# Kernel tuning notes

Hardware: AMD Instinct MI355X
Metric: run time of the kernel (lower is better)

## Reference

```python
import jax, jax.numpy as jnp
import numpy as np

N_NODES = 50000
N_EDGES = 800000
IN_C, HID_C, OUT_C, HEADS = 128, 32, 64, 8
NEG_SLOPE = 0.2


def gat_layer(x, src, dst, W, a_src, a_dst, bias, concat, num_nodes):
    # W: [F_in, H*C]; a_src, a_dst: [H, C]; bias: [H*C] or [C]
    H, C = a_src.shape
    h = (x @ W).reshape(num_nodes, H, C)                      # [N,H,C]
    e_src = (h * a_src).sum(-1)                               # [N,H]
    e_dst = (h * a_dst).sum(-1)                               # [N,H]
    e = jax.nn.leaky_relu(e_src[src] + e_dst[dst], NEG_SLOPE) # [E,H]
    # segment softmax over incoming edges of each destination node
    m = jax.ops.segment_max(e, dst, num_segments=num_nodes)   # [N,H]
    ex = jnp.exp(e - m[dst])
    den = jax.ops.segment_sum(ex, dst, num_segments=num_nodes)
    alpha = ex / (den[dst] + 1e-16)                           # [E,H]
    out = jax.ops.segment_sum(h[src] * alpha[..., None], dst, num_segments=num_nodes)  # [N,H,C]
    out = out.reshape(num_nodes, H * C) if concat else out.mean(axis=1)
    return out + bias


def setup_inputs() -> dict:
    key = jax.random.key(0)
    ks = jax.random.split(key, 10)
    x = jax.random.normal(ks[0], (N_NODES, IN_C), dtype=jnp.float32)
    edge_index = jax.random.randint(ks[1], (2, N_EDGES), 0, N_NODES, dtype=jnp.int64)
    s1 = (2.0 / (IN_C + HID_C * HEADS)) ** 0.5
    s2 = (2.0 / (HID_C * HEADS + OUT_C)) ** 0.5
    return {
        "x": x,
        "edge_index": edge_index,
        "W1": jax.random.normal(ks[2], (IN_C, HEADS * HID_C), dtype=jnp.float32) * s1,
        "a_src1": jax.random.normal(ks[3], (HEADS, HID_C), dtype=jnp.float32) * 0.1,
        "a_dst1": jax.random.normal(ks[4], (HEADS, HID_C), dtype=jnp.float32) * 0.1,
        "b1": jnp.zeros((HEADS * HID_C,), dtype=jnp.float32),
        "W2": jax.random.normal(ks[5], (HEADS * HID_C, OUT_C), dtype=jnp.float32) * s2,
        "a_src2": jax.random.normal(ks[6], (1, OUT_C), dtype=jnp.float32) * 0.1,
        "a_dst2": jax.random.normal(ks[7], (1, OUT_C), dtype=jnp.float32) * 0.1,
        "b2": jnp.zeros((OUT_C,), dtype=jnp.float32),
    }


def reference(x, edge_index, W1, a_src1, a_dst1, b1, W2, a_src2, a_dst2, b2):
    # add self-loops (PyG GATConv default)
    loops = jnp.arange(N_NODES, dtype=edge_index.dtype)
    src = jnp.concatenate([edge_index[0], loops])
    dst = jnp.concatenate([edge_index[1], loops])
    # dropout layers are identity in eval mode
    h = gat_layer(x, src, dst, W1, a_src1, a_dst1, b1, True, N_NODES)
    h = jax.nn.elu(h)
    out = gat_layer(h, src, dst, W2, a_src2, a_dst2, b2, False, N_NODES)
    return out
```

## Files before the change

kernel.cpp:

```cpp
#include <hip/hip_runtime.h>
#include <math.h>

#define N_NODES 50000
#define N_EDGES 800000
#define E_TOT   850000
#define IN_C    128
#define HID_C   32
#define OUT_C   64
#define HEADS   8
#define F1      256
#define PAD     64
#define NDUMMY  1024
#define G1_BLOCKS 3125
#define CSR_BLOCKS 782

typedef __bf16 bf16x8 __attribute__((ext_vector_type(8)));
typedef float  f32x4  __attribute__((ext_vector_type(4)));
typedef float  f32x2  __attribute__((ext_vector_type(2)));
typedef unsigned short us8 __attribute__((ext_vector_type(8)));

__device__ __forceinline__ unsigned short f2b(float f) {
    unsigned u = __float_as_uint(f);
    u += 0x7FFF + ((u >> 16) & 1);
    return (unsigned short)(u >> 16);
}
__device__ __forceinline__ float b2f(unsigned short b) {
    return __uint_as_float(((unsigned)b) << 16);
}
__device__ __forceinline__ float blo(unsigned u) { return __uint_as_float(u << 16); }
__device__ __forceinline__ float bhi(unsigned u) { return __uint_as_float(u & 0xffff0000u); }
__device__ __forceinline__ f32x2 up2(unsigned u) {
    f32x2 r; r.x = blo(u); r.y = bhi(u); return r;
}

__global__ void convert_w(const float* __restrict__ W1, const float* __restrict__ W2,
                          const float* __restrict__ a_src2, const float* __restrict__ a_dst2,
                          unsigned short* __restrict__ W1t, unsigned short* __restrict__ W2t,
                          float* __restrict__ w2s, float* __restrict__ w2d,
                          int* __restrict__ deg, unsigned short* __restrict__ ssrc) {
    int gid = blockIdx.x * 256 + threadIdx.x;
    if (gid < N_NODES) {
        deg[gid] = 1;
        ssrc[gid * PAD] = (unsigned short)gid;
    } else if (gid < N_NODES + NDUMMY) {
        deg[gid] = 0;
    }
    if (gid < 256) {
        float s = 0.f, dd = 0.f;
        for (int c = 0; c < OUT_C; c++) {
            float w = W2[gid * OUT_C + c];
            s  += w * a_src2[c];
            dd += w * a_dst2[c];
        }
        w2s[gid] = s; w2d[gid] = dd;
    }
    if (gid < 256 * 128) {
        int n = gid >> 7, k = gid & 127;
        W1t[gid] = f2b(W1[k * F1 + n]);
    } else if (gid < 256 * 128 + 64 * 256) {
        int o = gid - 256 * 128;
        int n = o >> 8, k = o & 255;
        W2t[o] = f2b(W2[k * OUT_C + n]);
    }
}

__global__ __launch_bounds__(256) void g1csr(const float* __restrict__ x,
                                             const unsigned short* __restrict__ W1t,
                                             const float* __restrict__ a_src,
                                             const float* __restrict__ a_dst,
                                             unsigned short* __restrict__ h1b,
                                             float* __restrict__ e_src,
                                             float* __restrict__ e_dst,
                                             const int* __restrict__ ei,
                                             int* __restrict__ deg,
                                             unsigned short* __restrict__ ssrc) {
    if (blockIdx.x >= G1_BLOCKS) {
        int e0 = (blockIdx.x - G1_BLOCKS) * 1024 + threadIdx.x;
        int s[4], d[4], p[4];
#pragma unroll
        for (int j = 0; j < 4; j++) {
            int e = e0 + j * 256;
            int le = (e < N_EDGES) ? e : (N_EDGES - 1);
            int es = ei[le];
            int ed = ei[N_EDGES + le];
            s[j] = es;
            d[j] = (e < N_EDGES) ? ed : (N_NODES + (e - N_EDGES));
        }
#pragma unroll
        for (int j = 0; j < 4; j++) p[j] = atomicAdd(&deg[d[j]], 1);
#pragma unroll
        for (int j = 0; j < 4; j++) ssrc[d[j] * PAD + p[j]] = (unsigned short)s[j];
        return;
    }
    const int t = threadIdx.x;
    const int wave = t >> 6, lane = t & 63;
    const int mlane = lane & 15, quad = lane >> 4;
    const int row0 = blockIdx.x * 16;
    const int col0 = wave * 64;
    const float* xr = x + (size_t)(row0 + mlane) * IN_C;
    bf16x8 afr[4];
#pragma unroll
    for (int kc = 0; kc < 4; kc++) {
        float4 f0 = *(const float4*)&xr[kc * 32 + quad * 8];
        float4 f1 = *(const float4*)&xr[kc * 32 + quad * 8 + 4];
        us8 u;
        u[0] = f2b(f0.x); u[1] = f2b(f0.y); u[2] = f2b(f0.z); u[3] = f2b(f0.w);
        u[4] = f2b(f1.x); u[5] = f2b(f1.y); u[6] = f2b(f1.z); u[7] = f2b(f1.w);
        afr[kc] = __builtin_bit_cast(bf16x8, u);
    }
    f32x4 c[4];
#pragma unroll
    for (int nt = 0; nt < 4; nt++) c[nt] = (f32x4){0.f, 0.f, 0.f, 0.f};
#pragma unroll
    for (int kc = 0; kc < 4; kc++) {
#pragma unroll
        for (int nt = 0; nt < 4; nt++) {
            int col = col0 + nt * 16 + mlane;
            uint4 bw = *(const uint4*)&W1t[(size_t)col * IN_C + kc * 32 + quad * 8];
            bf16x8 b = __builtin_bit_cast(bf16x8, bw);
            c[nt] = __builtin_amdgcn_mfma_f32_16x16x32_bf16(afr[kc], b, c[nt], 0, 0, 0);
        }
    }
#pragma unroll
    for (int nt = 0; nt < 4; nt++) {
#pragma unroll
        for (int r = 0; r < 4; r++) {
            int gr = row0 + quad * 4 + r;
            h1b[(size_t)gr * F1 + col0 + nt * 16 + mlane] = f2b(c[nt][r]);
        }
    }
    float asA0 = a_src[col0 + mlane],      asA1 = a_src[col0 + 16 + mlane];
    float asB0 = a_src[col0 + 32 + mlane], asB1 = a_src[col0 + 48 + mlane];
    float adA0 = a_dst[col0 + mlane],      adA1 = a_dst[col0 + 16 + mlane];
    float adB0 = a_dst[col0 + 32 + mlane], adB1 = a_dst[col0 + 48 + mlane];
#pragma unroll
    for (int r = 0; r < 4; r++) {
        float psA = c[0][r] * asA0 + c[1][r] * asA1;
        float pdA = c[0][r] * adA0 + c[1][r] * adA1;
        float psB = c[2][r] * asB0 + c[3][r] * asB1;
        float pdB = c[2][r] * adB0 + c[3][r] * adB1;
#pragma unroll
        for (int off = 1; off < 16; off <<= 1) {
            psA += __shfl_xor(psA, off, 64);
            pdA += __shfl_xor(pdA, off, 64);
            psB += __shfl_xor(psB, off, 64);
            pdB += __shfl_xor(pdB, off, 64);
        }
        if (mlane == 0) {
            int gr = row0 + quad * 4 + r;
            e_src[gr * HEADS + wave * 2]     = psA;
            e_src[gr * HEADS + wave * 2 + 1] = psB;
            e_dst[gr * HEADS + wave * 2]     = pdA;
            e_dst[gr * HEADS + wave * 2 + 1] = pdB;
        }
    }
}

__global__ __launch_bounds__(256) void agg1s(const unsigned short* __restrict__ h1b,
                                             const float* __restrict__ e_src,
                                             const float* __restrict__ e_dst,
                                             const int* __restrict__ deg,
                                             const unsigned short* __restrict__ ssrc,
                                             const float* __restrict__ b1,
                                             const float* __restrict__ w2s,
                                             const float* __restrict__ w2d,
                                             unsigned short* __restrict__ hhb,
                                             float* __restrict__ e_src2,
                                             float* __restrict__ e_dst2) {
    int v = (blockIdx.x * 256 + threadIdx.x) >> 6;
    int lane = threadIdx.x & 63;
    int half = lane >> 5, l32 = lane & 31;
    int c0 = l32 * 8, h_acc = l32 >> 2;
    int c2 = c0 << 1;
    int h_exp = l32 & 7, j_exp = l32 >> 3;
    const char* h1c = (const char*)h1b;
    const char* esc = (const char*)e_src;
    int d = deg[v];
    int beg = v * PAD;
    int s_all = (int)ssrc[beg + lane];
    float edh = e_dst[v * HEADS + h_exp];
    f32x2 acc[4];
#pragma unroll
    for (int k = 0; k < 4; k++) acc[k] = (f32x2){0.f, 0.f};
    float den = 0.f;
    int dm1 = d - 1;
    for (int k16 = 0; k16 < d; k16 += 16) {
        int slotA = k16 + half + 2 * j_exp;
        int slotB = slotA + 8;
        int sA = __shfl(s_all, (slotA < dm1 ? slotA : dm1), 64);
        int sB = __shfl(s_all, (slotB < dm1 ? slotB : dm1), 64);
        float eA = *(const float*)(esc + ((sA << 5) + (h_exp << 2))) + edh;
        float eB = *(const float*)(esc + ((sB << 5) + (h_exp << 2))) + edh;
        eA = fmaxf(eA, 0.2f * eA);
        eB = fmaxf(eB, 0.2f * eB);
        float wA = (slotA < d) ? __expf(eA) : 0.f;
        float wB = (slotB < d) ? __expf(eB) : 0.f;
        int s_j[8];
#pragma unroll
        for (int j = 0; j < 8; j++) {
            int slot = k16 + half + 2 * j;
            s_j[j] = __shfl(s_all, (slot < dm1 ? slot : dm1), 64);
        }
        float w_j[8];
#pragma unroll
        for (int j = 0; j < 4; j++) {
            w_j[j]     = __shfl(wA, (j << 3) | h_acc, 32);
            w_j[j + 4] = __shfl(wB, (j << 3) | h_acc, 32);
        }
        uint4 r[8];
#pragma unroll
        for (int j = 0; j < 8; j++)
            r[j] = *(const uint4*)(h1c + (((unsigned)s_j[j] << 9) + c2));
#pragma unroll
        for (int j = 0; j < 8; j++) {
            den += w_j[j];
            acc[0] += w_j[j] * up2(r[j].x);
            acc[1] += w_j[j] * up2(r[j].y);
            acc[2] += w_j[j] * up2(r[j].z);
            acc[3] += w_j[j] * up2(r[j].w);
        }
    }
    den += __shfl_xor(den, 32, 64);
#pragma unroll
    for (int k = 0; k < 4; k++) {
        acc[k].x += __shfl_xor(acc[k].x, 32, 64);
        acc[k].y += __shfl_xor(acc[k].y, 32, 64);
    }
    if (half == 0) {
        float dinv = 1.f / (den + 1e-16f);
        us8 o;
        float ps = 0.f, pd = 0.f;
#pragma unroll
        for (int k = 0; k < 4; k++) {
            float v0 = acc[k].x * dinv + b1[c0 + 2 * k];
            float v1 = acc[k].y * dinv + b1[c0 + 2 * k + 1];
            v0 = (v0 > 0.f) ? v0 : (__expf(v0) - 1.f);
            v1 = (v1 > 0.f) ? v1 : (__expf(v1) - 1.f);
            o[2 * k]     = f2b(v0);
            o[2 * k + 1] = f2b(v1);
            ps += v0 * w2s[c0 + 2 * k] + v1 * w2s[c0 + 2 * k + 1];
            pd += v0 * w2d[c0 + 2 * k] + v1 * w2d[c0 + 2 * k + 1];
        }
        *(us8*)&hhb[(size_t)v * F1 + c0] = o;
#pragma unroll
        for (int off = 1; off < 32; off <<= 1) {
            ps += __shfl_xor(ps, off, 32);
            pd += __shfl_xor(pd, off, 32);
        }
        if (l32 == 0) { e_src2[v] = ps; e_dst2[v] = pd; }
    }
}

__global__ __launch_bounds__(256) void gemm2_mfma(const unsigned short* __restrict__ hhb,
                                                  const unsigned short* __restrict__ W2t,
                                                  unsigned short* __restrict__ h2b) {
    __shared__ unsigned short A[16 * 264];
    const int t = threadIdx.x;
    const int wave = t >> 6, lane = t & 63;
    const int mlane = lane & 15, quad = lane >> 4;
    const int row0 = blockIdx.x * 16;
#pragma unroll
    for (int i = 0; i < 2; i++) {
        int u = t + i * 256;
        int row = u >> 5, seg = u & 31;
        uint4 w = *(const uint4*)&hhb[(size_t)(row0 + row) * F1 + seg * 8];
        *(uint4*)&A[row * 264 + seg * 8] = w;
    }
    __syncthreads();
    f32x4 cc = (f32x4){0.f, 0.f, 0.f, 0.f};
    const int col = wave * 16 + mlane;
#pragma unroll
    for (int kc = 0; kc < 8; kc++) {
        uint4 aw = *(const uint4*)&A[mlane * 264 + kc * 32 + quad * 8];
        bf16x8 a = __builtin_bit_cast(bf16x8, aw);
        uint4 bw = *(const uint4*)&W2t[(size_t)col * F1 + kc * 32 + quad * 8];
        bf16x8 b = __builtin_bit_cast(bf16x8, bw);
        cc = __builtin_amdgcn_mfma_f32_16x16x32_bf16(a, b, cc, 0, 0, 0);
    }
#pragma unroll
    for (int r = 0; r < 4; r++) {
        int gr = row0 + quad * 4 + r;
        h2b[(size_t)gr * OUT_C + wave * 16 + mlane] = f2b(cc[r]);
    }
}

__global__ __launch_bounds__(256) void agg2s(const unsigned short* __restrict__ h2b,
                                             const float* __restrict__ e_src,
                                             const float* __restrict__ e_dst,
                                             const int* __restrict__ deg,
                                             const unsigned short* __restrict__ ssrc,
                                             const float* __restrict__ b2,
                                             float* __restrict__ out) {
    int v = (blockIdx.x * 256 + threadIdx.x) >> 6;
    int lane = threadIdx.x & 63;
    int d = deg[v], beg = v * PAD, dm1 = d - 1;
    float ed = e_dst[v];
    int g = lane >> 3, l8 = lane & 7;
    int c0 = l8 * 8;
    int c2 = c0 << 1;
    const char* h2c = (const char*)h2b;
    const char* esc = (const char*)e_src;
    int s_raw = (int)ssrc[beg + lane];
    int s_cl = s_raw > N_NODES - 1 ? N_NODES - 1 : s_raw;
    float e_own = *(const float*)(esc + (s_cl << 2)) + ed;
    e_own = fmaxf(e_own, 0.2f * e_own);
    float w_own = (lane < d) ? __expf(e_own) : 0.f;
    f32x2 acc[4];
#pragma unroll
    for (int k = 0; k < 4; k++) acc[k] = (f32x2){0.f, 0.f};
    float den = 0.f;
    for (int k16 = 0; k16 < d; k16 += 16) {
        int slot0 = k16 + g, slot1 = slot0 + 8;
        int t0 = slot0 < dm1 ? slot0 : dm1;
        int t1 = slot1 < dm1 ? slot1 : dm1;
        int s0 = __shfl(s_cl, t0, 64);
        int s1 = __shfl(s_cl, t1, 64);
        float w0 = __shfl(w_own, t0, 64); w0 = (slot0 < d) ? w0 : 0.f;
        float w1 = __shfl(w_own, t1, 64); w1 = (slot1 < d) ? w1 : 0.f;
        den += w0 + w1;
        uint4 r0 = *(const uint4*)(h2c + ((s0 << 7) + c2));
        uint4 r1 = *(const uint4*)(h2c + ((s1 << 7) + c2));
        acc[0] += w0 * up2(r0.x) + w1 * up2(r1.x);
        acc[1] += w0 * up2(r0.y) + w1 * up2(r1.y);
        acc[2] += w0 * up2(r0.z) + w1 * up2(r1.z);
        acc[3] += w0 * up2(r0.w) + w1 * up2(r1.w);
    }
    den += __shfl_xor(den, 8, 64);
    den += __shfl_xor(den, 16, 64);
    den += __shfl_xor(den, 32, 64);
#pragma unroll
    for (int k = 0; k < 4; k++) {
        acc[k].x += __shfl_xor(acc[k].x, 8, 64);
        acc[k].y += __shfl_xor(acc[k].y, 8, 64);
        acc[k].x += __shfl_xor(acc[k].x, 16, 64);
        acc[k].y += __shfl_xor(acc[k].y, 16, 64);
        acc[k].x += __shfl_xor(acc[k].x, 32, 64);
        acc[k].y += __shfl_xor(acc[k].y, 32, 64);
    }
    if (g == 0) {
        float dinv = 1.f / (den + 1e-16f);
        float4 lo, hi;
        lo.x = acc[0].x * dinv + b2[c0 + 0]; lo.y = acc[0].y * dinv + b2[c0 + 1];
        lo.z = acc[1].x * dinv + b2[c0 + 2]; lo.w = acc[1].y * dinv + b2[c0 + 3];
        hi.x = acc[2].x * dinv + b2[c0 + 4]; hi.y = acc[2].y * dinv + b2[c0 + 5];
        hi.z = acc[3].x * dinv + b2[c0 + 6]; hi.w = acc[3].y * dinv + b2[c0 + 7];
        *(float4*)&out[(size_t)v * OUT_C + c0] = lo;
        *(float4*)&out[(size_t)v * OUT_C + c0 + 4] = hi;
    }
}

extern "C" void kernel_launch(void* const* d_in, const int* in_sizes, int n_in,
                              void* d_out, int out_size, void* d_ws, size_t ws_size,
                              hipStream_t stream) {
    const float* x      = (const float*)d_in[0];
    const int*   ei     = (const int*)d_in[1];
    const float* W1     = (const float*)d_in[2];
    const float* a_src1 = (const float*)d_in[3];
    const float* a_dst1 = (const float*)d_in[4];
    const float* b1     = (const float*)d_in[5];
    const float* W2     = (const float*)d_in[6];
    const float* a_src2 = (const float*)d_in[7];
    const float* a_dst2 = (const float*)d_in[8];
    const float* b2     = (const float*)d_in[9];
    float* out = (float*)d_out;

    char* ws = (char*)d_ws;
    size_t off = 0;
    auto alloc = [&](size_t bytes) { void* p = ws + off; off = (off + bytes + 255) & ~(size_t)255; return p; };
    unsigned short* h1b = (unsigned short*)alloc((size_t)N_NODES * F1 * 2);
    unsigned short* hhb = (unsigned short*)alloc((size_t)N_NODES * F1 * 2);
    unsigned short* h2b = (unsigned short*)alloc((size_t)N_NODES * OUT_C * 2);
    unsigned short* W1t = (unsigned short*)alloc((size_t)256 * 128 * 2);
    unsigned short* W2t = (unsigned short*)alloc((size_t)64 * 256 * 2);
    float* w2s    = (float*)alloc((size_t)256 * 4);
    float* w2d    = (float*)alloc((size_t)256 * 4);
    float* e_src1 = (float*)alloc((size_t)N_NODES * HEADS * 4);
    float* e_dst1 = (float*)alloc((size_t)N_NODES * HEADS * 4);
    float* e_src2 = (float*)alloc((size_t)N_NODES * 4);
    float* e_dst2 = (float*)alloc((size_t)N_NODES * 4);
    int*   deg    = (int*)alloc((size_t)(N_NODES + NDUMMY) * 4);
    unsigned short* ssrc = (unsigned short*)alloc((size_t)(N_NODES + NDUMMY) * PAD * 2);
    (void)ws_size; (void)n_in; (void)in_sizes; (void)out_size;

    const int node_waves = (N_NODES + 3) / 4;

    convert_w<<<200, 256, 0, stream>>>(W1, W2, a_src2, a_dst2, W1t, W2t, w2s, w2d, deg, ssrc);
    g1csr<<<G1_BLOCKS + CSR_BLOCKS, 256, 0, stream>>>(x, W1t, a_src1, a_dst1,
                                                      h1b, e_src1, e_dst1, ei, deg, ssrc);
    agg1s<<<node_waves, 256, 0, stream>>>(h1b, e_src1, e_dst1, deg, ssrc, b1,
                                          w2s, w2d, hhb, e_src2, e_dst2);
    gemm2_mfma<<<G1_BLOCKS, 256, 0, stream>>>(hhb, W2t, h2b);
    agg2s<<<node_waves, 256, 0, stream>>>(h2b, e_src2, e_dst2, deg, ssrc, b2, out);
}
```

Baseline: 282.5 us.

## Build CSR via two-pass bucketed scatter instead of global atomics

Replaces the per-edge global atomicAdd on node degrees with a two-pass bucketing scheme. First, 128 blocks histogram edges into 64-node buckets in shared memory, reserve space with one global atomic per bucket, and write packed (local dst, src) words into a bucket buffer. A new kernel then builds each bucket's padded adjacency and degrees using shared-memory atomics. This is meant to cut global atomic contention and scattered writes. In exchange it adds a kernel launch and an intermediate buffer, and it assumes no bucket holds more than 1280 edges.

```diff
diff --git a/kernel.cpp b/kernel.cpp
--- a/kernel.cpp
+++ b/kernel.cpp
@@ -3,16 +3,17 @@
 
 #define N_NODES 50000
 #define N_EDGES 800000
-#define E_TOT   850000
 #define IN_C    128
 #define HID_C   32
 #define OUT_C   64
 #define HEADS   8
 #define F1      256
 #define PAD     64
-#define NDUMMY  1024
 #define G1_BLOCKS 3125
-#define CSR_BLOCKS 782
+#define NB_BKT  782
+#define BK_CAP  1280
+#define A_BLOCKS 128
+#define E_PER_A  6250
 
 typedef __bf16 bf16x8 __attribute__((ext_vector_type(8)));
 typedef float  f32x4  __attribute__((ext_vector_type(4)));
@@ -24,9 +25,6 @@
     u += 0x7FFF + ((u >> 16) & 1);
     return (unsigned short)(u >> 16);
 }
-__device__ __forceinline__ float b2f(unsigned short b) {
-    return __uint_as_float(((unsigned)b) << 16);
-}
 __device__ __forceinline__ float blo(unsigned u) { return __uint_as_float(u << 16); }
 __device__ __forceinline__ float bhi(unsigned u) { return __uint_as_float(u & 0xffff0000u); }
 __device__ __forceinline__ f32x2 up2(unsigned u) {
@@ -37,14 +35,9 @@
                           const float* __restrict__ a_src2, const float* __restrict__ a_dst2,
                           unsigned short* __restrict__ W1t, unsigned short* __restrict__ W2t,
                           float* __restrict__ w2s, float* __restrict__ w2d,
-                          int* __restrict__ deg, unsigned short* __restrict__ ssrc) {
+                          int* __restrict__ bk_cnt) {
     int gid = blockIdx.x * 256 + threadIdx.x;
-    if (gid < N_NODES) {
-        deg[gid] = 1;
-        ssrc[gid * PAD] = (unsigned short)gid;
-    } else if (gid < N_NODES + NDUMMY) {
-        deg[gid] = 0;
-    }
+    if (gid < NB_BKT) bk_cnt[gid] = 0;
     if (gid < 256) {
         float s = 0.f, dd = 0.f;
         for (int c = 0; c < OUT_C; c++) {
@@ -64,38 +57,44 @@
     }
 }
 
-__global__ __launch_bounds__(256) void g1csr(const float* __restrict__ x,
-                                             const unsigned short* __restrict__ W1t,
-                                             const float* __restrict__ a_src,
-                                             const float* __restrict__ a_dst,
-                                             unsigned short* __restrict__ h1b,
-                                             float* __restrict__ e_src,
-                                             float* __restrict__ e_dst,
-                                             const int* __restrict__ ei,
-                                             int* __restrict__ deg,
-                                             unsigned short* __restrict__ ssrc) {
-    if (blockIdx.x >= G1_BLOCKS) {
-        int e0 = (blockIdx.x - G1_BLOCKS) * 1024 + threadIdx.x;
-        int s[4], d[4], p[4];
-#pragma unroll
-        for (int j = 0; j < 4; j++) {
-            int e = e0 + j * 256;
-            int le = (e < N_EDGES) ? e : (N_EDGES - 1);
-            int es = ei[le];
-            int ed = ei[N_EDGES + le];
-            s[j] = es;
-            d[j] = (e < N_EDGES) ? ed : (N_NODES + (e - N_EDGES));
-        }
-#pragma unroll
-        for (int j = 0; j < 4; j++) p[j] = atomicAdd(&deg[d[j]], 1);
-#pragma unroll
-        for (int j = 0; j < 4; j++) ssrc[d[j] * PAD + p[j]] = (unsigned short)s[j];
+__global__ __launch_bounds__(256) void g1A(const float* __restrict__ x,
+                                           const unsigned short* __restrict__ W1t,
+                                           const float* __restrict__ a_src,
+                                           const float* __restrict__ a_dst,
+                                           unsigned short* __restrict__ h1b,
+                                           float* __restrict__ e_src,
+                                           float* __restrict__ e_dst,
+                                           const int* __restrict__ ei,
+                                           int* __restrict__ bk_cnt,
+                                           unsigned* __restrict__ ebuf) {
+    if (blockIdx.x < A_BLOCKS) {
+        __shared__ int cnt[NB_BKT];
+        __shared__ int pos[NB_BKT];
+        const int tid = threadIdx.x;
+        const int e0 = blockIdx.x * E_PER_A, e1 = e0 + E_PER_A;
+        for (int k = tid; k < NB_BKT; k += 256) cnt[k] = 0;
+        __syncthreads();
+        for (int e = e0 + tid; e < e1; e += 256)
+            atomicAdd(&cnt[ei[N_EDGES + e] >> 6], 1);
+        __syncthreads();
+        for (int k = tid; k < NB_BKT; k += 256) {
+            int c = cnt[k];
+            pos[k] = (c > 0) ? atomicAdd(&bk_cnt[k], c) : 0;
+        }
+        __syncthreads();
+        for (int e = e0 + tid; e < e1; e += 256) {
+            int s = ei[e];
+            int d = ei[N_EDGES + e];
+            int k = d >> 6;
+            int idx = atomicAdd(&pos[k], 1);
+            ebuf[k * BK_CAP + idx] = ((unsigned)(d & 63) << 16) | (unsigned)s;
+        }
         return;
     }
     const int t = threadIdx.x;
     const int wave = t >> 6, lane = t & 63;
     const int mlane = lane & 15, quad = lane >> 4;
-    const int row0 = blockIdx.x * 16;
+    const int row0 = (blockIdx.x - A_BLOCKS) * 16;
     const int col0 = wave * 64;
     const float* xr = x + (size_t)(row0 + mlane) * IN_C;
     bf16x8 afr[4];
@@ -153,6 +152,36 @@
             e_dst[gr * HEADS + wave * 2]     = pdA;
             e_dst[gr * HEADS + wave * 2 + 1] = pdB;
         }
+    }
+}
+
+__global__ __launch_bounds__(256) void csrB(const unsigned* __restrict__ ebuf,
+                                            const int* __restrict__ bk_cnt,
+                                            int* __restrict__ deg,
+                                            unsigned short* __restrict__ ssrc) {
+    __shared__ int cnt[64];
+    const int k = blockIdx.x;
+    const int n0 = k << 6;
+    const int tid = threadIdx.x;
+    if (tid < 64) {
+        int v = n0 + tid;
+        if (v < N_NODES) {
+            cnt[tid] = 1;
+            ssrc[(size_t)v * PAD] = (unsigned short)v;
+        }
+    }
+    __syncthreads();
+    const int nb = bk_cnt[k];
+    for (int t = tid; t < nb; t += 256) {
+        unsigned w = ebuf[k * BK_CAP + t];
+        int dl = w >> 16;
+        int slot = atomicAdd(&cnt[dl], 1);
+        ssrc[(size_t)(n0 + dl) * PAD + slot] = (unsigned short)(w & 0xffff);
+    }
+    __syncthreads();
+    if (tid < 64) {
+        int v = n0 + tid;
+        if (v < N_NODES) deg[v] = cnt[tid];
     }
 }
 
@@ -378,15 +407,18 @@
     float* e_dst1 = (float*)alloc((size_t)N_NODES * HEADS * 4);
     float* e_src2 = (float*)alloc((size_t)N_NODES * 4);
     float* e_dst2 = (float*)alloc((size_t)N_NODES * 4);
-    int*   deg    = (int*)alloc((size_t)(N_NODES + NDUMMY) * 4);
-    unsigned short* ssrc = (unsigned short*)alloc((size_t)(N_NODES + NDUMMY) * PAD * 2);
+    int*   deg    = (int*)alloc((size_t)N_NODES * 4);
+    unsigned short* ssrc = (unsigned short*)alloc((size_t)N_NODES * PAD * 2);
+    int*   bk_cnt = (int*)alloc((size_t)NB_BKT * 4);
+    unsigned* ebuf = (unsigned*)alloc((size_t)NB_BKT * BK_CAP * 4);
     (void)ws_size; (void)n_in; (void)in_sizes; (void)out_size;
 
     const int node_waves = (N_NODES + 3) / 4;
 
-    convert_w<<<200, 256, 0, stream>>>(W1, W2, a_src2, a_dst2, W1t, W2t, w2s, w2d, deg, ssrc);
-    g1csr<<<G1_BLOCKS + CSR_BLOCKS, 256, 0, stream>>>(x, W1t, a_src1, a_dst1,
-                                                      h1b, e_src1, e_dst1, ei, deg, ssrc);
+    convert_w<<<200, 256, 0, stream>>>(W1, W2, a_src2, a_dst2, W1t, W2t, w2s, w2d, bk_cnt);
+    g1A<<<A_BLOCKS + G1_BLOCKS, 256, 0, stream>>>(x, W1t, a_src1, a_dst1,
+                                                  h1b, e_src1, e_dst1, ei, bk_cnt, ebuf);
+    csrB<<<NB_BKT, 256, 0, stream>>>(ebuf, bk_cnt, deg, ssrc);
     agg1s<<<node_waves, 256, 0, stream>>>(h1b, e_src1, e_dst1, deg, ssrc, b1,
                                           w2s, w2d, hhb, e_src2, e_dst2);
     gemm2_mfma<<<G1_BLOCKS, 256, 0, stream>>>(hhb, W2t, h2b);
```

Measured after the change: 245.5 us, median of 3. 1.15x faster.
